# Kernel optimization log

Hardware: AMD Instinct MI355X
Metric: run time of the kernel (lower is better)

The kernel has to match this reference:

```python
import jax, jax.numpy as jnp
import numpy as np

B, LQ, LK, D, H = 8, 1024, 1024, 1024, 8
DH = D // H  # per-head dim (att_units // num_heads, and V head dim since V = k)
LN_EPS = 1e-5


def setup_inputs() -> dict:
    key = jax.random.key(0)
    ks = jax.random.split(key, 8)
    s = 1.0 / np.sqrt(D)
    return {
        "q": jax.random.normal(ks[0], (B, LQ, D), dtype=jnp.float32),
        "k": jax.random.normal(ks[1], (B, LK, D), dtype=jnp.float32),
        "Wq": jax.random.normal(ks[2], (D, D), dtype=jnp.float32) * s,
        "bq": jnp.zeros((D,), dtype=jnp.float32),
        "Wk": jax.random.normal(ks[3], (D, D), dtype=jnp.float32) * s,
        "bk": jnp.zeros((D,), dtype=jnp.float32),
        "ln_gamma": jnp.ones((D,), dtype=jnp.float32),
        "ln_beta": jnp.zeros((D,), dtype=jnp.float32),
    }


def _layer_norm(x, gamma, beta):
    mu = jnp.mean(x, axis=-1, keepdims=True)
    var = jnp.mean(jnp.square(x - mu), axis=-1, keepdims=True)
    return (x - mu) * jax.lax.rsqrt(var + LN_EPS) * gamma + beta


def reference(q, k, Wq, bq, Wk, bk, ln_gamma, ln_beta):
    # q: [B, LQ, D], k: [B, LK, D]
    Q = q @ Wq + bq                      # [B, LQ, D]
    K = k @ Wk + bk                      # [B, LK, D]
    V = k                                # V is the raw key input (no projection)
    Qh = Q.reshape(B, LQ, H, DH)         # split(att_units//H, -1)+concat(0) == head reshape
    Kh = K.reshape(B, LK, H, DH)
    Vh = V.reshape(B, LK, H, DH)
    sim = jnp.einsum("bqhd,bkhd->bhqk", Qh, Kh) / np.sqrt(DH).astype(np.float32)
    attn = jax.nn.softmax(sim, axis=-1)  # [B, H, LQ, LK]
    att_h = jnp.einsum("bhqk,bkhd->bqhd", attn, Vh).reshape(B, LQ, D)
    att_h = att_h * 0.1 + q * 0.9        # residual blend
    att_h = _layer_norm(att_h, ln_gamma, ln_beta)
    return att_h  # ff_units_list == [] -> ff is None -> ff_h = att_h
```

## Files before the change

kernel.cpp:

```cpp
#include <hip/hip_runtime.h>
#include <hip/hip_bf16.h>
#include <cstdint>

#define BATCH 8
#define SEQ   1024
#define DMODEL 1024
#define NHEAD 8
#define DHEAD 128

using short8 = __attribute__((ext_vector_type(8))) short;
using f32x4  = __attribute__((ext_vector_type(4))) float;
typedef unsigned short u16;

__device__ inline u16 f2bf(float f) {
    union { float f; uint32_t u; } v; v.f = f;
    uint32_t r = (v.u + 0x7FFFu + ((v.u >> 16) & 1u)) >> 16;
    return (u16)r;
}

#define GLL16(g, l)                                                                        \
    __builtin_amdgcn_global_load_lds((__attribute__((address_space(1))) const uint32_t*)(g), \
                                     (__attribute__((address_space(3))) uint32_t*)(l), 16, 0, 0)

__global__ __launch_bounds__(256) void conv_bf16(const float* __restrict__ q,
                                                 const float* __restrict__ kin,
                                                 u16* __restrict__ dst) {
    size_t e = ((size_t)blockIdx.x * 256 + threadIdx.x) * 8;
    const size_t N1 = (size_t)8 * 1024 * 1024;
    const float* s = (e < N1) ? (q + e) : (kin + (e - N1));
    float4 a = *(const float4*)s;
    float4 b = *(const float4*)(s + 4);
    uint4 r;
    r.x = (uint32_t)f2bf(a.x) | ((uint32_t)f2bf(a.y) << 16);
    r.y = (uint32_t)f2bf(a.z) | ((uint32_t)f2bf(a.w) << 16);
    r.z = (uint32_t)f2bf(b.x) | ((uint32_t)f2bf(b.y) << 16);
    r.w = (uint32_t)f2bf(b.z) | ((uint32_t)f2bf(b.w) << 16);
    *(uint4*)(dst + e) = r;
}

__global__ void transpose_conv(const float* __restrict__ Wq,
                               const float* __restrict__ Wk,
                               const float* __restrict__ kin,
                               u16* __restrict__ WqT,
                               u16* __restrict__ WkT,
                               u16* __restrict__ Vt) {
    __shared__ float tile[32][33];
    int z = blockIdx.z;
    const float* src;
    u16* dst;
    if (z == 0)      { src = Wq; dst = WqT; }
    else if (z == 1) { src = Wk; dst = WkT; }
    else {
        src = kin + (size_t)(z - 2) * DMODEL * SEQ;
        dst = Vt  + (size_t)(z - 2) * DMODEL * SEQ;
    }
    int x  = blockIdx.x * 32 + threadIdx.x;
    int y0 = blockIdx.y * 32;
    for (int i = threadIdx.y; i < 32; i += 8)
        tile[i][threadIdx.x] = src[(size_t)(y0 + i) * 1024 + x];
    __syncthreads();
    int xo  = y0 + threadIdx.x;
    int yo0 = blockIdx.x * 32;
    for (int i = threadIdx.y; i < 32; i += 8)
        dst[(size_t)(yo0 + i) * 1024 + xo] = f2bf(tile[threadIdx.x][i]);
}

__global__ __launch_bounds__(256, 4) void gemm_bias(const u16* __restrict__ A,
                                                    const u16* __restrict__ BT,
                                                    const float* __restrict__ bias,
                                                    u16* __restrict__ Out,
                                                    float scale) {
    __shared__ __align__(16) u16 As[2][128 * 32];
    __shared__ __align__(16) u16 Bs[2][128 * 32];

    int bid = blockIdx.x;
    int swz = (bid & 7) * 64 + (bid >> 3);
    int mt = swz >> 3, nt = swz & 7;
    int m0 = mt * 128, n0 = nt * 128;

    int t = threadIdx.x, lane = t & 63, w = t >> 6;
    int wm = w >> 1, wn = w & 1;
    int lr = lane & 15, lg = lane >> 4;

    const u16* pa[2];
    const u16* pb[2];
#pragma unroll
    for (int i = 0; i < 2; ++i) {
        int L = (w * 2 + i) * 64 + lane;
        int rp = L >> 3, ss = L & 7;
        int u = ss ^ (rp & 7);
        int row = (rp << 1) | (u >> 2);
        int g = u & 3;
        pa[i] = A  + (size_t)(m0 + row) * 1024 + g * 8;
        pb[i] = BT + (size_t)(n0 + row) * 1024 + g * 8;
    }
    int aoff[4], boff[4];
#pragma unroll
    for (int f = 0; f < 4; ++f) {
        int rowA = wm * 64 + f * 16 + lr;
        int sA = (((rowA & 1) << 2) | lg) ^ ((rowA >> 1) & 7);
        aoff[f] = (rowA >> 1) * 64 + sA * 8;
        int rowB = wn * 64 + f * 16 + lr;
        int sB = (((rowB & 1) << 2) | lg) ^ ((rowB >> 1) & 7);
        boff[f] = (rowB >> 1) * 64 + sB * 8;
    }

    f32x4 acc[4][4] = {};

#define GSTAGE(buf)                                         \
    {                                                       \
        _Pragma("unroll")                                   \
        for (int i = 0; i < 2; ++i) {                       \
            GLL16(pa[i], &As[buf][(w * 2 + i) * 512]);      \
            GLL16(pb[i], &Bs[buf][(w * 2 + i) * 512]);      \
            pa[i] += 32;                                    \
            pb[i] += 32;                                    \
        }                                                   \
    }

    GSTAGE(0);
    __syncthreads();

    int cur = 0;
    for (int k0 = 0; k0 < DMODEL; k0 += 32) {
        if (k0 + 32 < DMODEL) GSTAGE(cur ^ 1);
        short8 af[4], bfr[4];
#pragma unroll
        for (int f = 0; f < 4; ++f) {
            af[f]  = *(const short8*)&As[cur][aoff[f]];
            bfr[f] = *(const short8*)&Bs[cur][boff[f]];
        }
        __builtin_amdgcn_s_setprio(1);
#pragma unroll
        for (int fm = 0; fm < 4; ++fm)
#pragma unroll
            for (int fn = 0; fn < 4; ++fn)
                acc[fm][fn] = __builtin_amdgcn_mfma_f32_16x16x32_bf16(af[fm], bfr[fn], acc[fm][fn], 0, 0, 0);
        __builtin_amdgcn_s_setprio(0);
        __syncthreads();
        cur ^= 1;
    }
#undef GSTAGE

#pragma unroll
    for (int fn = 0; fn < 4; ++fn) {
        int col = n0 + wn * 64 + fn * 16 + lr;
        float bv = bias[col];
#pragma unroll
        for (int fm = 0; fm < 4; ++fm)
#pragma unroll
            for (int j = 0; j < 4; ++j) {
                int row = m0 + wm * 64 + fm * 16 + lg * 4 + j;
                Out[(size_t)row * 1024 + col] = f2bf((acc[fm][fn][j] + bv) * scale);
            }
    }
}

__global__ __launch_bounds__(512, 4) void attn_kernel(const u16* __restrict__ Qb,
                                                      const u16* __restrict__ Kb,
                                                      const u16* __restrict__ Vt,
                                                      float* __restrict__ AO) {
    __shared__ __align__(16) u16 Kbuf[2][64 * 128];
    __shared__ __align__(16) u16 Vbuf[2][128 * 64];
    __shared__ __align__(16) u16 Pl[8][16 * 64];

    int bid = blockIdx.x;
    int swz = (bid & 7) * 64 + (bid >> 3);
    int bh  = swz >> 3;
    int qt  = swz & 7;
    int b = bh >> 3, h = bh & 7;
    int q0 = qt * 128;

    int t = threadIdx.x, lane = t & 63, w = t >> 6;
    int lr = lane & 15, lg = lane >> 4;

    short8 qf[4];
    {
        size_t qbase = (size_t)(b * SEQ + q0 + w * 16 + lr) * 1024 + h * DHEAD;
#pragma unroll
        for (int kk = 0; kk < 4; ++kk)
            qf[kk] = *(const short8*)&Qb[qbase + kk * 32 + lg * 8];
    }

    float m_i = -1e30f, l_i = 0.f;
    f32x4 o[8] = {};
    u16* Pw = &Pl[w][0];
    const int pwrow = lr * 64;
    const int lx = lr & 7;

#define STAGE(nb, kk0)                                                                   \
    {                                                                                    \
        _Pragma("unroll")                                                                \
        for (int i = 0; i < 2; ++i) {                                                    \
            int g = (w * 2 + i) * 64 + lane;                                             \
            int row = g >> 4, cp = g & 15;                                               \
            int c = cp ^ (row & 7);                                                      \
            const u16* src = Kb + ((size_t)(b * SEQ + (kk0) + row) * 1024 + h * 128 + c * 8); \
            GLL16(src, &Kbuf[nb][(w * 2 + i) * 512]);                                    \
        }                                                                                \
        _Pragma("unroll")                                                                \
        for (int i = 0; i < 2; ++i) {                                                    \
            int g = (w * 2 + i) * 64 + lane;                                             \
            int d = g >> 3, cp = g & 7;                                                  \
            int c = cp ^ (d & 7);                                                        \
            const u16* src = Vt + ((size_t)(bh * 128 + d) * 1024 + (kk0) + c * 8);       \
            GLL16(src, &Vbuf[nb][(w * 2 + i) * 512]);                                    \
        }                                                                                \
    }

    STAGE(0, 0);
    __syncthreads();

    int cur = 0;
    for (int k0 = 0; k0 < SEQ; k0 += 64) {
        if (k0 + 64 < SEQ) STAGE(cur ^ 1, k0 + 64);

        const u16* Kc = &Kbuf[cur][0];
        f32x4 s[4] = {};
        __builtin_amdgcn_s_setprio(1);
#pragma unroll
        for (int fn = 0; fn < 4; ++fn) {
            int krow = (fn * 16 + lr) * 128;
#pragma unroll
            for (int kk = 0; kk < 4; ++kk) {
                short8 kf = *(const short8*)&Kc[krow + (((kk * 4 + lg) ^ lx) << 3)];
                s[fn] = __builtin_amdgcn_mfma_f32_16x16x32_bf16(kf, qf[kk], s[fn], 0, 0, 0);
            }
        }
        __builtin_amdgcn_s_setprio(0);

        float pmax = s[0][0];
#pragma unroll
        for (int fn = 0; fn < 4; ++fn)
#pragma unroll
            for (int j = 0; j < 4; ++j) pmax = fmaxf(pmax, s[fn][j]);
        pmax = fmaxf(pmax, __shfl_xor(pmax, 16));
        pmax = fmaxf(pmax, __shfl_xor(pmax, 32));

        if (__any(pmax > m_i + 8.f)) {
            float mnew = fmaxf(m_i, pmax);
            float alpha = __expf(m_i - mnew);
            m_i = mnew;
            l_i *= alpha;
#pragma unroll
            for (int db = 0; db < 8; ++db) o[db] *= alpha;
        }

        float p[4][4];
        float lsum = 0.f;
#pragma unroll
        for (int fn = 0; fn < 4; ++fn)
#pragma unroll
            for (int j = 0; j < 4; ++j) {
                p[fn][j] = __expf(s[fn][j] - m_i);
                lsum += p[fn][j];
            }
        lsum += __shfl_xor(lsum, 16);
        lsum += __shfl_xor(lsum, 32);
        l_i += lsum;

#pragma unroll
        for (int fn = 0; fn < 4; ++fn) {
            uint2 pk;
            pk.x = (uint32_t)f2bf(p[fn][0]) | ((uint32_t)f2bf(p[fn][1]) << 16);
            pk.y = (uint32_t)f2bf(p[fn][2]) | ((uint32_t)f2bf(p[fn][3]) << 16);
            int idx = pwrow + (((fn * 2 + (lg >> 1)) ^ lx) << 3) + ((lg & 1) << 2);
            *(uint2*)&Pw[idx] = pk;
        }

        const u16* Vc = &Vbuf[cur][0];
        short8 pf0 = *(const short8*)&Pw[pwrow + ((lg ^ lx) << 3)];
        short8 pf1 = *(const short8*)&Pw[pwrow + (((4 + lg) ^ lx) << 3)];
        __builtin_amdgcn_s_setprio(1);
#pragma unroll
        for (int db = 0; db < 8; ++db) {
            int vr = (db * 16 + lr) * 64;
            short8 v0 = *(const short8*)&Vc[vr + ((lg ^ lx) << 3)];
            short8 v1 = *(const short8*)&Vc[vr + (((4 + lg) ^ lx) << 3)];
            o[db] = __builtin_amdgcn_mfma_f32_16x16x32_bf16(v0, pf0, o[db], 0, 0, 0);
            o[db] = __builtin_amdgcn_mfma_f32_16x16x32_bf16(v1, pf1, o[db], 0, 0, 0);
        }
        __builtin_amdgcn_s_setprio(0);

        __syncthreads();
        cur ^= 1;
    }

    float inv = 1.f / l_i;
    size_t obase = (size_t)(b * SEQ + q0 + w * 16 + lr) * 1024 + h * DHEAD + lg * 4;
#pragma unroll
    for (int db = 0; db < 8; ++db) {
        float4 ov;
        ov.x = o[db][0] * inv;
        ov.y = o[db][1] * inv;
        ov.z = o[db][2] * inv;
        ov.w = o[db][3] * inv;
        *(float4*)&AO[obase + db * 16] = ov;
    }
#undef STAGE
}

__global__ __launch_bounds__(256) void ln_kernel(float* __restrict__ AO,
                                                 const float* __restrict__ qin,
                                                 const float* __restrict__ gamma,
                                                 const float* __restrict__ beta,
                                                 float* __restrict__ out) {
    __shared__ float red[8];
    int row = blockIdx.x;
    int t = threadIdx.x;
    size_t base = (size_t)row * 1024 + t * 4;

    float4 a = *(const float4*)&AO[base];
    float4 qq = *(const float4*)&qin[base];
    float x0 = a.x * 0.1f + qq.x * 0.9f;
    float x1 = a.y * 0.1f + qq.y * 0.9f;
    float x2 = a.z * 0.1f + qq.z * 0.9f;
    float x3 = a.w * 0.1f + qq.w * 0.9f;

    float s  = x0 + x1 + x2 + x3;
    float s2 = x0 * x0 + x1 * x1 + x2 * x2 + x3 * x3;
    for (int d = 1; d < 64; d <<= 1) {
        s  += __shfl_xor(s, d);
        s2 += __shfl_xor(s2, d);
    }
    int w = t >> 6, lane = t & 63;
    if (lane == 0) { red[w] = s; red[4 + w] = s2; }
    __syncthreads();
    s  = red[0] + red[1] + red[2] + red[3];
    s2 = red[4] + red[5] + red[6] + red[7];

    float mu   = s * (1.f / 1024.f);
    float var  = s2 * (1.f / 1024.f) - mu * mu;
    float rstd = rsqrtf(var + 1e-5f);

    float4 g  = *(const float4*)&gamma[t * 4];
    float4 be = *(const float4*)&beta[t * 4];
    float4 o;
    o.x = (x0 - mu) * rstd * g.x + be.x;
    o.y = (x1 - mu) * rstd * g.y + be.y;
    o.z = (x2 - mu) * rstd * g.z + be.z;
    o.w = (x3 - mu) * rstd * g.w + be.w;
    *(float4*)&out[base] = o;
}

extern "C" void kernel_launch(void* const* d_in, const int* in_sizes, int n_in,
                              void* d_out, int out_size, void* d_ws, size_t ws_size,
                              hipStream_t stream) {
    const float* q     = (const float*)d_in[0];
    const float* k     = (const float*)d_in[1];
    const float* Wq    = (const float*)d_in[2];
    const float* bq    = (const float*)d_in[3];
    const float* Wk    = (const float*)d_in[4];
    const float* bk    = (const float*)d_in[5];
    const float* gamma = (const float*)d_in[6];
    const float* beta  = (const float*)d_in[7];
    float* out = (float*)d_out;

    char* ws = (char*)d_ws;
    u16* WqT = (u16*)ws;
    u16* WkT = (u16*)(ws + (size_t)(2  << 20));
    u16* Qb  = (u16*)(ws + (size_t)(4  << 20));
    u16* Kb  = (u16*)(ws + (size_t)(20 << 20));
    u16* Vt  = (u16*)(ws + (size_t)(36 << 20));

    u16* qkb = (u16*)d_out;

    conv_bf16<<<8192, 256, 0, stream>>>(q, k, qkb);

    transpose_conv<<<dim3(32, 32, 2 + BATCH), dim3(32, 8), 0, stream>>>(Wq, Wk, k, WqT, WkT, Vt);

    gemm_bias<<<512, 256, 0, stream>>>(qkb, WqT, bq, Qb, 0.08838834764831845f);
    gemm_bias<<<512, 256, 0, stream>>>(qkb + (size_t)8 * 1024 * 1024, WkT, bk, Kb, 1.0f);

    attn_kernel<<<512, 512, 0, stream>>>(Qb, Kb, Vt, out);

    ln_kernel<<<8192, 256, 0, stream>>>(out, q, gamma, beta, out);
}
```

Measured before the change: 151.4 us.

## Merge Q/K projections into one launch, fuse k bf16 conversion, use exp2 softmax

Result: faster. 135.1 us (-10.8%).

```diff
diff --git a/kernel.cpp b/kernel.cpp
--- a/kernel.cpp
+++ b/kernel.cpp
@@ -18,18 +18,23 @@
     return (u16)r;
 }
 
+__device__ inline float exp2_fast(float x) { return __builtin_amdgcn_exp2f(x); }
+
+__device__ inline uint32_t cvtpk_bf16(float a, float b) {
+    uint32_t r;
+    asm("v_cvt_pk_bf16_f32 %0, %1, %2" : "=v"(r) : "v"(a), "v"(b));
+    return r;
+}
+
 #define GLL16(g, l)                                                                        \
     __builtin_amdgcn_global_load_lds((__attribute__((address_space(1))) const uint32_t*)(g), \
                                      (__attribute__((address_space(3))) uint32_t*)(l), 16, 0, 0)
 
 __global__ __launch_bounds__(256) void conv_bf16(const float* __restrict__ q,
-                                                 const float* __restrict__ kin,
                                                  u16* __restrict__ dst) {
     size_t e = ((size_t)blockIdx.x * 256 + threadIdx.x) * 8;
-    const size_t N1 = (size_t)8 * 1024 * 1024;
-    const float* s = (e < N1) ? (q + e) : (kin + (e - N1));
-    float4 a = *(const float4*)s;
-    float4 b = *(const float4*)(s + 4);
+    float4 a = *(const float4*)(q + e);
+    float4 b = *(const float4*)(q + e + 4);
     uint4 r;
     r.x = (uint32_t)f2bf(a.x) | ((uint32_t)f2bf(a.y) << 16);
     r.y = (uint32_t)f2bf(a.z) | ((uint32_t)f2bf(a.w) << 16);
@@ -43,21 +48,27 @@
                                const float* __restrict__ kin,
                                u16* __restrict__ WqT,
                                u16* __restrict__ WkT,
-                               u16* __restrict__ Vt) {
+                               u16* __restrict__ Vt,
+                               u16* __restrict__ kb) {
     __shared__ float tile[32][33];
     int z = blockIdx.z;
     const float* src;
     u16* dst;
+    u16* sdst = nullptr;
     if (z == 0)      { src = Wq; dst = WqT; }
     else if (z == 1) { src = Wk; dst = WkT; }
     else {
-        src = kin + (size_t)(z - 2) * DMODEL * SEQ;
-        dst = Vt  + (size_t)(z - 2) * DMODEL * SEQ;
+        src  = kin + (size_t)(z - 2) * DMODEL * SEQ;
+        dst  = Vt  + (size_t)(z - 2) * DMODEL * SEQ;
+        sdst = kb  + (size_t)(z - 2) * DMODEL * SEQ;
     }
     int x  = blockIdx.x * 32 + threadIdx.x;
     int y0 = blockIdx.y * 32;
-    for (int i = threadIdx.y; i < 32; i += 8)
-        tile[i][threadIdx.x] = src[(size_t)(y0 + i) * 1024 + x];
+    for (int i = threadIdx.y; i < 32; i += 8) {
+        float v = src[(size_t)(y0 + i) * 1024 + x];
+        tile[i][threadIdx.x] = v;
+        if (sdst) sdst[(size_t)(y0 + i) * 1024 + x] = f2bf(v);
+    }
     __syncthreads();
     int xo  = y0 + threadIdx.x;
     int yo0 = blockIdx.x * 32;
@@ -65,16 +76,27 @@
         dst[(size_t)(yo0 + i) * 1024 + xo] = f2bf(tile[threadIdx.x][i]);
 }
 
-__global__ __launch_bounds__(256, 4) void gemm_bias(const u16* __restrict__ A,
-                                                    const u16* __restrict__ BT,
-                                                    const float* __restrict__ bias,
-                                                    u16* __restrict__ Out,
-                                                    float scale) {
+__global__ __launch_bounds__(256, 4) void gemm_dual(const u16* __restrict__ Aq,
+                                                    const u16* __restrict__ Ak,
+                                                    const u16* __restrict__ BTq,
+                                                    const u16* __restrict__ BTk,
+                                                    const float* __restrict__ biasq,
+                                                    const float* __restrict__ biask,
+                                                    u16* __restrict__ Outq,
+                                                    u16* __restrict__ Outk) {
     __shared__ __align__(16) u16 As[2][128 * 32];
     __shared__ __align__(16) u16 Bs[2][128 * 32];
 
     int bid = blockIdx.x;
-    int swz = (bid & 7) * 64 + (bid >> 3);
+    int half = bid >> 9;
+    int b2 = bid & 511;
+    const u16* A  = half ? Ak  : Aq;
+    const u16* BT = half ? BTk : BTq;
+    const float* bias = half ? biask : biasq;
+    u16* Out = half ? Outk : Outq;
+    float scale = half ? 1.0f : (0.08838834764831845f * 1.4426950408889634f);
+
+    int swz = (b2 & 7) * 64 + (b2 >> 3);
     int mt = swz >> 3, nt = swz & 7;
     int m0 = mt * 128, n0 = nt * 128;
 
@@ -237,9 +259,9 @@
         pmax = fmaxf(pmax, __shfl_xor(pmax, 16));
         pmax = fmaxf(pmax, __shfl_xor(pmax, 32));
 
-        if (__any(pmax > m_i + 8.f)) {
+        if (__any(pmax > m_i + 11.5416f)) {
             float mnew = fmaxf(m_i, pmax);
-            float alpha = __expf(m_i - mnew);
+            float alpha = exp2_fast(m_i - mnew);
             m_i = mnew;
             l_i *= alpha;
 #pragma unroll
@@ -252,7 +274,7 @@
         for (int fn = 0; fn < 4; ++fn)
 #pragma unroll
             for (int j = 0; j < 4; ++j) {
-                p[fn][j] = __expf(s[fn][j] - m_i);
+                p[fn][j] = exp2_fast(s[fn][j] - m_i);
                 lsum += p[fn][j];
             }
         lsum += __shfl_xor(lsum, 16);
@@ -262,8 +284,8 @@
 #pragma unroll
         for (int fn = 0; fn < 4; ++fn) {
             uint2 pk;
-            pk.x = (uint32_t)f2bf(p[fn][0]) | ((uint32_t)f2bf(p[fn][1]) << 16);
-            pk.y = (uint32_t)f2bf(p[fn][2]) | ((uint32_t)f2bf(p[fn][3]) << 16);
+            pk.x = cvtpk_bf16(p[fn][0], p[fn][1]);
+            pk.y = cvtpk_bf16(p[fn][2], p[fn][3]);
             int idx = pwrow + (((fn * 2 + (lg >> 1)) ^ lx) << 3) + ((lg & 1) << 2);
             *(uint2*)&Pw[idx] = pk;
         }
@@ -363,14 +385,14 @@
     u16* Kb  = (u16*)(ws + (size_t)(20 << 20));
     u16* Vt  = (u16*)(ws + (size_t)(36 << 20));
 
-    u16* qkb = (u16*)d_out;
-
-    conv_bf16<<<8192, 256, 0, stream>>>(q, k, qkb);
-
-    transpose_conv<<<dim3(32, 32, 2 + BATCH), dim3(32, 8), 0, stream>>>(Wq, Wk, k, WqT, WkT, Vt);
-
-    gemm_bias<<<512, 256, 0, stream>>>(qkb, WqT, bq, Qb, 0.08838834764831845f);
-    gemm_bias<<<512, 256, 0, stream>>>(qkb + (size_t)8 * 1024 * 1024, WkT, bk, Kb, 1.0f);
+    u16* qb = (u16*)d_out;
+    u16* kb = qb + (size_t)8 * 1024 * 1024;
+
+    conv_bf16<<<4096, 256, 0, stream>>>(q, qb);
+
+    transpose_conv<<<dim3(32, 32, 2 + BATCH), dim3(32, 8), 0, stream>>>(Wq, Wk, k, WqT, WkT, Vt, kb);
+
+    gemm_dual<<<1024, 256, 0, stream>>>(qb, kb, WqT, WkT, bq, bk, Qb, Kb);
 
     attn_kernel<<<512, 512, 0, stream>>>(Qb, Kb, Vt, out);
 
```
